# Kernel tuning notes

Hardware: AMD Instinct MI355X
Metric: run time of the kernel (lower is better)

The kernel has to match this reference:

```python
import jax, jax.numpy as jnp
import numpy as np

N, F_IN, D, R, E = 50000, 128, 96, 2, 800000


def setup_inputs() -> dict:
    key = jax.random.key(0)
    ks = jax.random.split(key, 8)
    sc = lambda k, shape: jax.random.normal(k, shape, jnp.float32) * 0.05
    return {
        "x": jax.random.normal(ks[0], (N, F_IN), jnp.float32),
        "edge_index": jax.random.randint(ks[1], (2, E), 0, N),
        "edge_attr": jax.random.uniform(ks[2], (E, R), dtype=jnp.float32),
        # nn.Linear(F_IN, D)
        "Wf": sc(ks[3], (D, F_IN)),
        "bf": jnp.zeros((D,), jnp.float32),
        # RGCNConv: per-relation weights, root weight, bias
        "W": sc(ks[4], (R, D, D)),
        "root": sc(ks[5], (D, D)),
        "bias": jnp.zeros((D,), jnp.float32),
    }


def _rgcn_conv(h, src, dst, etype, W, root, bias):
    # PyG RGCNConv (no bases/blocks, aggr='mean'):
    #   out = x @ root + bias + sum_r mean_{edges of type r}(x[src]) @ W[r]
    msg = h[src]  # [E, D] gather
    out = h @ root + bias
    for r in range(R):
        w = (etype == r).astype(h.dtype)[:, None]  # [E, 1] relation mask
        s = jax.ops.segment_sum(msg * w, dst, num_segments=N)   # [N, D] scatter-add
        cnt = jax.ops.segment_sum(w, dst, num_segments=N)       # [N, 1]
        agg = s / jnp.maximum(cnt, 1.0)                          # mean, safe for deg 0
        out = out + agg @ W[r]
    return out


def reference(x, edge_index, edge_attr, Wf, bf, W, root, bias):
    src, dst = edge_index[0], edge_index[1]
    etype = jnp.argmax(edge_attr, axis=1)  # [E]
    h = jax.nn.relu(x @ Wf.T + bf)
    for _ in range(3):
        h = jax.nn.relu(_rgcn_conv(h, src, dst, etype, W, root, bias))
    return h
```

## Files before the change

### kernel.cpp

```cpp
#include <hip/hip_runtime.h>

#define DN 96
#define FIN 128

typedef unsigned int uint_t;
typedef unsigned short ushort_t;

typedef __attribute__((ext_vector_type(8))) short short8v;
typedef __attribute__((ext_vector_type(4))) float f32x4;

#define MFMA16 __builtin_amdgcn_mfma_f32_16x16x32_bf16

struct __align__(4) U3 { uint_t x, y, z; };

__device__ __forceinline__ ushort_t f2bf(float f) {
    uint_t u = __float_as_uint(f);
    uint_t r = (u + 0x7FFFu + ((u >> 16) & 1u)) >> 16;
    return (ushort_t)r;
}
__device__ __forceinline__ float bf2f(ushort_t h) { return __uint_as_float(((uint_t)h) << 16); }
__device__ __forceinline__ float bf_lo(uint_t u) { return __uint_as_float(u << 16); }
__device__ __forceinline__ float bf_hi(uint_t u) { return __uint_as_float(u & 0xFFFF0000u); }

__device__ __forceinline__ U3 ldrow(const uint_t* __restrict__ g, int idx, int j) {
    return *(const U3*)(g + (size_t)idx * 48 + 3 * j);
}
__device__ __forceinline__ void acc6(float* s, U3 v) {
    s[0] += bf_lo(v.x); s[1] += bf_hi(v.x);
    s[2] += bf_lo(v.y); s[3] += bf_hi(v.y);
    s[4] += bf_lo(v.z); s[5] += bf_hi(v.z);
}


__global__ __launch_bounds__(256) void prep_kernel(
    const int* __restrict__ ei, const float* __restrict__ ea,
    uint_t* __restrict__ kdx, uint_t* __restrict__ kdy,
    const float* __restrict__ root, const float* __restrict__ W, const float* __restrict__ Wf,
    ushort_t* __restrict__ Bph, ushort_t* __restrict__ Bpl,
    ushort_t* __restrict__ Wfh, ushort_t* __restrict__ Wfl,
    ushort_t* g0A, ushort_t* g1A, ushort_t* g0B, ushort_t* g1B,
    int E, int N, int KD_BLKS)
{
    int bid = blockIdx.x;
    int t = threadIdx.x;
    if (bid < KD_BLKS) {
        int e = bid * 256 + t;
        if (e < E) {
            int src = ei[e];
            int dst = ei[E + e];
            float2 a = *(const float2*)(ea + 2 * e);
            int r = (a.y > a.x) ? 1 : 0;
            kdx[e] = (uint_t)dst | ((uint_t)r << 16);
            kdy[e] = (uint_t)src;
        }
    } else if (bid < KD_BLKS + 78) {
        if (t >= 64) return;
        int l = t;
        int fid = bid - KD_BLKS;
        if (fid < 54) {
            int ct = fid / 3, ks = fid % 3;
            int mat = ct / 6, cw = ct % 6;
            const float* M = (mat == 0) ? root : (W + (size_t)(mat - 1) * DN * DN);
            int k0 = 32 * ks + (l >> 4) * 8;
            int col = 16 * cw + (l & 15);
#pragma unroll
            for (int j = 0; j < 8; j++) {
                float v = M[(size_t)(k0 + j) * DN + col];
                ushort_t h = f2bf(v);
                size_t idx = ((size_t)fid * 64 + l) * 8 + j;
                Bph[idx] = h;
                Bpl[idx] = f2bf(v - bf2f(h));
            }
        } else {
            int f2 = fid - 54;
            int ct = f2 >> 2, ks = f2 & 3;
            int k0 = 32 * ks + (l >> 4) * 8;
            int col = 16 * ct + (l & 15);
#pragma unroll
            for (int j = 0; j < 8; j++) {
                float v = Wf[(size_t)col * FIN + k0 + j];
                ushort_t h = f2bf(v);
                size_t idx = ((size_t)f2 * 64 + l) * 8 + j;
                Wfh[idx] = h;
                Wfl[idx] = f2bf(v - bf2f(h));
            }
        }
    } else {
        int pair = bid - (KD_BLKS + 78);
        ushort_t* ga = pair ? g0B : g0A;
        ushort_t* gb = pair ? g1B : g1A;
        if (t < 96) ga[(size_t)N * DN + t] = 0;
        else if (t < 192) gb[(size_t)N * DN + (t - 96)] = 0;
    }
}


__global__ __launch_bounds__(256) void hist_part(const uint_t* __restrict__ kdx,
                                                 int* __restrict__ cnt, int E, int N, int PS) {
    int p = blockIdx.x & 7;
    int c = blockIdx.x >> 3;
    int base = c * 2048 + threadIdx.x;
#pragma unroll
    for (int i = 0; i < 8; i++) {
        int e = base + i * 256;
        if (e < E) {
            uint_t v = kdx[e];
            int dst = v & 0xFFFF;
            if (dst / PS == p) {
                int r = (v >> 16) & 1;
                atomicAdd(&cnt[r * N + dst], 1);
            }
        }
    }
}

__global__ void offsets_kernel(const int* __restrict__ cnt, int* __restrict__ total,
                               int* __restrict__ rowstart, int* __restrict__ fillptr,
                               int nbins) {
    __shared__ int sd[256];
    __shared__ int sbase;
    int t = threadIdx.x;
    int b = blockIdx.x * 256 + t;
    int v = (b < nbins) ? cnt[b] : 0;
    sd[t] = v;
    __syncthreads();
    for (int off = 1; off < 256; off <<= 1) {
        int add = (t >= off) ? sd[t - off] : 0;
        __syncthreads();
        sd[t] += add;
        __syncthreads();
    }
    if (t == 255) sbase = atomicAdd(total, sd[255]);
    __syncthreads();
    if (b < nbins) {
        int s = sbase + sd[t] - v;
        rowstart[b] = s;
        fillptr[b] = s;
    }
}


__device__ __forceinline__ void cvt8(float4 x, float4 y, short8v& hi, short8v& lo) {
    union { short8v v; ushort_t u[8]; } H, L;
    float f[8] = {x.x, x.y, x.z, x.w, y.x, y.y, y.z, y.w};
#pragma unroll
    for (int j = 0; j < 8; j++) {
        ushort_t h = f2bf(f[j]);
        H.u[j] = h;
        L.u[j] = f2bf(f[j] - bf2f(h));
    }
    hi = H.v; lo = L.v;
}


__global__ __launch_bounds__(256) void fill_lin(
    const uint_t* __restrict__ kdx, const uint_t* __restrict__ kdy,
    int* __restrict__ fillptr, int* __restrict__ srcs,
    const float* __restrict__ xin,
    const ushort_t* __restrict__ WfH, const ushort_t* __restrict__ WfL,
    const ushort_t* __restrict__ Bph, const ushort_t* __restrict__ Bpl,
    const float* __restrict__ bfv, const float* __restrict__ bias,
    float* __restrict__ hrootOut, ushort_t* __restrict__ g0Out, ushort_t* __restrict__ g1Out,
    int E, int N, int PS, int FILL_BLKS)
{
    __shared__ float sout[4][16][100];
    int t = threadIdx.x;

    if (blockIdx.x < FILL_BLKS) {
        int p = blockIdx.x & 7;
        int c = blockIdx.x >> 3;
        int base = c * 2048 + t;
#pragma unroll
        for (int i = 0; i < 8; i++) {
            int e = base + i * 256;
            if (e < E) {
                uint_t v = kdx[e];
                int dst = v & 0xFFFF;
                if (dst / PS == p) {
                    int r = (v >> 16) & 1;
                    int pos = atomicAdd(&fillptr[r * N + dst], 1);
                    srcs[pos] = (int)kdy[e];
                }
            }
        }
        return;
    }

    int bid2 = blockIdx.x - FILL_BLKS;
    int l = t & 63;
    int w = t >> 6;

    int slab = bid2 * 64 + w * 16;
    int row = slab + (l & 15);
    if (row >= N) row = N - 1;
    const float* xrow = xin + (size_t)row * FIN + ((l >> 4) * 8);
    short8v ah4[4], al4[4];
#pragma unroll
    for (int ks = 0; ks < 4; ks++) {
        float4 xa = *(const float4*)(xrow + 32 * ks);
        float4 xb = *(const float4*)(xrow + 32 * ks + 4);
        cvt8(xa, xb, ah4[ks], al4[ks]);
    }
#pragma unroll
    for (int ct = 0; ct < 6; ct++) {
        f32x4 hh = {0.f,0.f,0.f,0.f}, hl_ = {0.f,0.f,0.f,0.f}, lh = {0.f,0.f,0.f,0.f};
#pragma unroll
        for (int ks = 0; ks < 4; ks++) {
            size_t base = ((size_t)(ct * 4 + ks) * 64 + l) * 8;
            short8v bh = *(const short8v*)(WfH + base);
            short8v bl = *(const short8v*)(WfL + base);
            hh  = MFMA16(ah4[ks], bh, hh, 0, 0, 0);
            hl_ = MFMA16(ah4[ks], bl, hl_, 0, 0, 0);
            lh  = MFMA16(al4[ks], bh, lh, 0, 0, 0);
        }
        f32x4 acc = hh + hl_ + lh;
        int col = ct * 16 + (l & 15);
        float bv = bfv[col];
        int lr0 = (l >> 4) * 4;
#pragma unroll
        for (int r = 0; r < 4; r++) {
            float v = acc[r] + bv;
            sout[w][lr0 + r][col] = v > 0.f ? v : 0.f;
        }
    }
    __syncthreads();

    const float* srow = &sout[w][l & 15][0];
    int mbase = bid2 * 64 + w * 16 + ((l >> 4) << 2);
    int k0 = (l >> 4) * 8;
    short8v ah[3], al[3];
#pragma unroll
    for (int ks = 0; ks < 3; ks++) {
        float4 xa = *(const float4*)(srow + k0 + 32 * ks);
        float4 xb = *(const float4*)(srow + k0 + 32 * ks + 4);
        cvt8(xa, xb, ah[ks], al[ks]);
    }
    for (int ct = 0; ct < 18; ct++) {
        f32x4 hh = {0.f,0.f,0.f,0.f}, hl_ = {0.f,0.f,0.f,0.f}, lh = {0.f,0.f,0.f,0.f};
#pragma unroll
        for (int ks = 0; ks < 3; ks++) {
            size_t base = ((size_t)(ct * 3 + ks) * 64 + l) * 8;
            short8v bh = *(const short8v*)(Bph + base);
            short8v bl = *(const short8v*)(Bpl + base);
            hh  = MFMA16(ah[ks], bh, hh, 0, 0, 0);
            hl_ = MFMA16(ah[ks], bl, hl_, 0, 0, 0);
            lh  = MFMA16(al[ks], bh, lh, 0, 0, 0);
        }
        f32x4 acc = hh + hl_ + lh;
        int mat = ct / 6;
        int col = (ct % 6) * 16 + (l & 15);
        if (mat == 0) {
            float bv = bias[col];
#pragma unroll
            for (int r = 0; r < 4; r++) {
                int m = mbase + r;
                if (m < N) hrootOut[(size_t)m * DN + col] = acc[r] + bv;
            }
        } else {
            ushort_t* g = (mat == 1) ? g0Out : g1Out;
#pragma unroll
            for (int r = 0; r < 4; r++) {
                int m = mbase + r;
                if (m < N) g[(size_t)m * DN + col] = f2bf(acc[r]);
            }
        }
    }
}


template <int GEMM>
__global__ __launch_bounds__(256) void layer_kernel(
    const float* __restrict__ hrootIn,
    const uint_t* __restrict__ g0In, const uint_t* __restrict__ g1In,
    const int* __restrict__ rowstart, const int* __restrict__ cnt,
    const int* __restrict__ srcs,
    const ushort_t* __restrict__ Bph, const ushort_t* __restrict__ Bpl,
    const float* __restrict__ bias,
    float* __restrict__ hrootOut, ushort_t* __restrict__ g0Out, ushort_t* __restrict__ g1Out,
    float* __restrict__ dout, int N)
{
    __shared__ float sout[16][100];
    int t = threadIdx.x;

    {
        int grp = t >> 4;
        int j = t & 15;
        int n = blockIdx.x * 16 + grp;
        bool valid = n < N;
        int nc = valid ? n : N - 1;

        const float* hr = hrootIn + (size_t)nc * DN + 6 * j;
        float2 p0 = *(const float2*)hr;
        float2 p1 = *(const float2*)(hr + 2);
        float2 p2 = *(const float2*)(hr + 4);

        float a[6] = {0.f,0.f,0.f,0.f,0.f,0.f};
#pragma unroll
        for (int r = 0; r < 2; r++) {
            int c    = valid ? cnt[r * N + nc] : 0;
            int base = valid ? rowstart[r * N + nc] : 0;
            const uint_t* g = r ? g1In : g0In;
            const int* sp = srcs + base;
            float sA[6] = {0.f,0.f,0.f,0.f,0.f,0.f};
            float sB[6] = {0.f,0.f,0.f,0.f,0.f,0.f};
            for (int e = 0; e < c; e += 8) {
                int i0 = (e + 0 < c) ? sp[e + 0] : N;
                int i1 = (e + 1 < c) ? sp[e + 1] : N;
                int i2 = (e + 2 < c) ? sp[e + 2] : N;
                int i3 = (e + 3 < c) ? sp[e + 3] : N;
                int i4 = (e + 4 < c) ? sp[e + 4] : N;
                int i5 = (e + 5 < c) ? sp[e + 5] : N;
                int i6 = (e + 6 < c) ? sp[e + 6] : N;
                int i7 = (e + 7 < c) ? sp[e + 7] : N;
                U3 v0 = ldrow(g, i0, j);
                U3 v1 = ldrow(g, i1, j);
                U3 v2 = ldrow(g, i2, j);
                U3 v3 = ldrow(g, i3, j);
                U3 v4 = ldrow(g, i4, j);
                U3 v5 = ldrow(g, i5, j);
                U3 v6 = ldrow(g, i6, j);
                U3 v7 = ldrow(g, i7, j);
                acc6(sA, v0); acc6(sB, v1); acc6(sA, v2); acc6(sB, v3);
                acc6(sA, v4); acc6(sB, v5); acc6(sA, v6); acc6(sB, v7);
            }
            float inv = (c > 0) ? 1.f / (float)c : 0.f;
#pragma unroll
            for (int k = 0; k < 6; k++) a[k] += (sA[k] + sB[k]) * inv;
        }
        float o0 = fmaxf(p0.x + a[0], 0.f);
        float o1 = fmaxf(p0.y + a[1], 0.f);
        float o2 = fmaxf(p1.x + a[2], 0.f);
        float o3 = fmaxf(p1.y + a[3], 0.f);
        float o4 = fmaxf(p2.x + a[4], 0.f);
        float o5 = fmaxf(p2.y + a[5], 0.f);
        if constexpr (GEMM) {
            float* dr = &sout[grp][6 * j];
            dr[0]=o0; dr[1]=o1; dr[2]=o2; dr[3]=o3; dr[4]=o4; dr[5]=o5;
        } else {
            if (valid) {
                float* dr = dout + (size_t)n * DN + 6 * j;
                *(float2*)(dr)     = make_float2(o0, o1);
                *(float2*)(dr + 2) = make_float2(o2, o3);
                *(float2*)(dr + 4) = make_float2(o4, o5);
            }
        }
    }

    if constexpr (!GEMM) return;
    __syncthreads();

    {
        int l = t & 63;
        int w = t >> 6;
        const float* srow = &sout[l & 15][0];
        int mbase = blockIdx.x * 16 + ((l >> 4) << 2);
        int k0 = (l >> 4) * 8;
        short8v ah[3], al[3];
#pragma unroll
        for (int ks = 0; ks < 3; ks++) {
            float4 xa = *(const float4*)(srow + k0 + 32 * ks);
            float4 xb = *(const float4*)(srow + k0 + 32 * ks + 4);
            cvt8(xa, xb, ah[ks], al[ks]);
        }
        int ctS, ctC;
        ctS = (w < 2) ? 5 * w : 10 + 4 * (w - 2);
        ctC = (w < 2) ? 5 : 4;
        for (int ci = 0; ci < ctC; ci++) {
            int ct = ctS + ci;
            f32x4 hh = {0.f,0.f,0.f,0.f}, hl_ = {0.f,0.f,0.f,0.f}, lh = {0.f,0.f,0.f,0.f};
#pragma unroll
            for (int ks = 0; ks < 3; ks++) {
                size_t base = ((size_t)(ct * 3 + ks) * 64 + l) * 8;
                short8v bh = *(const short8v*)(Bph + base);
                short8v bl = *(const short8v*)(Bpl + base);
                hh  = MFMA16(ah[ks], bh, hh, 0, 0, 0);
                hl_ = MFMA16(ah[ks], bl, hl_, 0, 0, 0);
                lh  = MFMA16(al[ks], bh, lh, 0, 0, 0);
            }
            f32x4 acc = hh + hl_ + lh;
            int mat = ct / 6;
            int col = (ct % 6) * 16 + (l & 15);
            if (mat == 0) {
                float bv = bias[col];
#pragma unroll
                for (int r = 0; r < 4; r++) {
                    int m = mbase + r;
                    if (m < N) hrootOut[(size_t)m * DN + col] = acc[r] + bv;
                }
            } else {
                ushort_t* g = (mat == 1) ? g0Out : g1Out;
#pragma unroll
                for (int r = 0; r < 4; r++) {
                    int m = mbase + r;
                    if (m < N) g[(size_t)m * DN + col] = f2bf(acc[r]);
                }
            }
        }
    }
}

extern "C" void kernel_launch(void* const* d_in, const int* in_sizes, int n_in,
                              void* d_out, int out_size, void* d_ws, size_t ws_size,
                              hipStream_t stream) {
    const float* x    = (const float*)d_in[0];
    const int*   ei   = (const int*)d_in[1];
    const float* ea   = (const float*)d_in[2];
    const float* Wf   = (const float*)d_in[3];
    const float* bf   = (const float*)d_in[4];
    const float* W    = (const float*)d_in[5];
    const float* root = (const float*)d_in[6];
    const float* bias = (const float*)d_in[7];
    float* out = (float*)d_out;

    int N = in_sizes[0] / FIN;
    int E = in_sizes[1] / 2;
    int nbins = 2 * N;
    int PS = (N + 7) / 8;
    size_t NR = (size_t)(N + 1) * DN;

    int* cnt      = (int*)d_ws;
    int* total    = cnt + nbins;
    int* rowstart = cnt + nbins + 4;
    int* fillptr  = rowstart + nbins;
    int* srcs     = fillptr + nbins;
    uint_t* kdx   = (uint_t*)(srcs + E);
    uint_t* kdy   = kdx + E;
    ushort_t* Bph = (ushort_t*)(kdy + E);
    ushort_t* Bpl = Bph + 54 * 512;
    ushort_t* Wfh = Bpl + 54 * 512;
    ushort_t* Wfl = Wfh + 24 * 512;
    float* hrootA = (float*)(Wfl + 24 * 512);
    ushort_t* g0A = (ushort_t*)(hrootA + (size_t)N * DN);
    ushort_t* g1A = g0A + NR;
    float* hrootB = (float*)(g1A + NR);
    ushort_t* g0B = (ushort_t*)(hrootB + (size_t)N * DN);
    ushort_t* g1B = g0B + NR;

    hipMemsetAsync(cnt, 0, (size_t)(nbins + 1) * sizeof(int), stream);

    int KD_BLKS = (E + 255) / 256;
    int nchunk = (E + 2047) / 2048;
    int FILL_BLKS = nchunk * 8;
    int blk64 = (N + 63) / 64;
    int blk16 = (N + 15) / 16;

    prep_kernel<<<KD_BLKS + 78 + 2, 256, 0, stream>>>(
        ei, ea, kdx, kdy, root, W, Wf, Bph, Bpl, Wfh, Wfl,
        g0A, g1A, g0B, g1B, E, N, KD_BLKS);
    hist_part<<<FILL_BLKS, 256, 0, stream>>>(kdx, cnt, E, N, PS);
    offsets_kernel<<<(nbins + 255) / 256, 256, 0, stream>>>(cnt, total, rowstart, fillptr, nbins);
    fill_lin<<<FILL_BLKS + blk64, 256, 0, stream>>>(
        kdx, kdy, fillptr, srcs, x, Wfh, Wfl, Bph, Bpl, bf, bias,
        hrootA, g0A, g1A, E, N, PS, FILL_BLKS);
    layer_kernel<1><<<blk16, 256, 0, stream>>>(
        hrootA, (const uint_t*)g0A, (const uint_t*)g1A, rowstart, cnt, srcs,
        Bph, Bpl, bias, hrootB, g0B, g1B, nullptr, N);
    layer_kernel<1><<<blk16, 256, 0, stream>>>(
        hrootB, (const uint_t*)g0B, (const uint_t*)g1B, rowstart, cnt, srcs,
        Bph, Bpl, bias, hrootA, g0A, g1A, nullptr, N);
    layer_kernel<0><<<blk16, 256, 0, stream>>>(
        hrootA, (const uint_t*)g0A, (const uint_t*)g1A, rowstart, cnt, srcs,
        nullptr, nullptr, nullptr, nullptr, nullptr, nullptr, out, N);
}
```

Before: 278.9 us.

## Store edge sources as 16-bit and split fill from linear GEMM kernel

Edge source indices (kdy and the CSR srcs array) are stored as 16-bit values instead of 32-bit, halving the bytes for index writes and reads in the fill pass and in all three gather layers. The fused fill+linear kernel is split into two separate launches, fill_part and lin_gemm. This removes the mixed-role grid but adds a launch and loses overlap between the scatter and the GEMM. The 16-bit indices only hold for N below 65536, which the task's N=50000 satisfies, as does the existing dst packing.

```diff
diff --git a/kernel.cpp b/kernel.cpp
--- a/kernel.cpp
+++ b/kernel.cpp
@@ -34,7 +34,7 @@
 
 __global__ __launch_bounds__(256) void prep_kernel(
     const int* __restrict__ ei, const float* __restrict__ ea,
-    uint_t* __restrict__ kdx, uint_t* __restrict__ kdy,
+    uint_t* __restrict__ kdx, ushort_t* __restrict__ kdy,
     const float* __restrict__ root, const float* __restrict__ W, const float* __restrict__ Wf,
     ushort_t* __restrict__ Bph, ushort_t* __restrict__ Bpl,
     ushort_t* __restrict__ Wfh, ushort_t* __restrict__ Wfl,
@@ -51,7 +51,7 @@
             float2 a = *(const float2*)(ea + 2 * e);
             int r = (a.y > a.x) ? 1 : 0;
             kdx[e] = (uint_t)dst | ((uint_t)r << 16);
-            kdy[e] = (uint_t)src;
+            kdy[e] = (ushort_t)src;
         }
     } else if (bid < KD_BLKS + 78) {
         if (t >= 64) return;
@@ -140,6 +140,29 @@
 }
 
 
+__global__ __launch_bounds__(256) void fill_part(const uint_t* __restrict__ kdx,
+                            const ushort_t* __restrict__ kdy,
+                            int* __restrict__ fillptr, ushort_t* __restrict__ srcs,
+                            int E, int N, int PS) {
+    int p = blockIdx.x & 7;
+    int c = blockIdx.x >> 3;
+    int base = c * 2048 + threadIdx.x;
+#pragma unroll
+    for (int i = 0; i < 8; i++) {
+        int e = base + i * 256;
+        if (e < E) {
+            uint_t v = kdx[e];
+            int dst = v & 0xFFFF;
+            if (dst / PS == p) {
+                int r = (v >> 16) & 1;
+                int pos = atomicAdd(&fillptr[r * N + dst], 1);
+                srcs[pos] = kdy[e];
+            }
+        }
+    }
+}
+
+
 __device__ __forceinline__ void cvt8(float4 x, float4 y, short8v& hi, short8v& lo) {
     union { short8v v; ushort_t u[8]; } H, L;
     float f[8] = {x.x, x.y, x.z, x.w, y.x, y.y, y.z, y.w};
@@ -153,44 +176,20 @@
 }
 
 
-__global__ __launch_bounds__(256) void fill_lin(
-    const uint_t* __restrict__ kdx, const uint_t* __restrict__ kdy,
-    int* __restrict__ fillptr, int* __restrict__ srcs,
+__global__ __launch_bounds__(256) void lin_gemm(
     const float* __restrict__ xin,
     const ushort_t* __restrict__ WfH, const ushort_t* __restrict__ WfL,
     const ushort_t* __restrict__ Bph, const ushort_t* __restrict__ Bpl,
     const float* __restrict__ bfv, const float* __restrict__ bias,
     float* __restrict__ hrootOut, ushort_t* __restrict__ g0Out, ushort_t* __restrict__ g1Out,
-    int E, int N, int PS, int FILL_BLKS)
+    int N)
 {
     __shared__ float sout[4][16][100];
     int t = threadIdx.x;
-
-    if (blockIdx.x < FILL_BLKS) {
-        int p = blockIdx.x & 7;
-        int c = blockIdx.x >> 3;
-        int base = c * 2048 + t;
-#pragma unroll
-        for (int i = 0; i < 8; i++) {
-            int e = base + i * 256;
-            if (e < E) {
-                uint_t v = kdx[e];
-                int dst = v & 0xFFFF;
-                if (dst / PS == p) {
-                    int r = (v >> 16) & 1;
-                    int pos = atomicAdd(&fillptr[r * N + dst], 1);
-                    srcs[pos] = (int)kdy[e];
-                }
-            }
-        }
-        return;
-    }
-
-    int bid2 = blockIdx.x - FILL_BLKS;
     int l = t & 63;
     int w = t >> 6;
 
-    int slab = bid2 * 64 + w * 16;
+    int slab = blockIdx.x * 64 + w * 16;
     int row = slab + (l & 15);
     if (row >= N) row = N - 1;
     const float* xrow = xin + (size_t)row * FIN + ((l >> 4) * 8);
@@ -226,7 +225,7 @@
     __syncthreads();
 
     const float* srow = &sout[w][l & 15][0];
-    int mbase = bid2 * 64 + w * 16 + ((l >> 4) << 2);
+    int mbase = blockIdx.x * 64 + w * 16 + ((l >> 4) << 2);
     int k0 = (l >> 4) * 8;
     short8v ah[3], al[3];
 #pragma unroll
@@ -273,7 +272,7 @@
     const float* __restrict__ hrootIn,
     const uint_t* __restrict__ g0In, const uint_t* __restrict__ g1In,
     const int* __restrict__ rowstart, const int* __restrict__ cnt,
-    const int* __restrict__ srcs,
+    const ushort_t* __restrict__ srcs,
     const ushort_t* __restrict__ Bph, const ushort_t* __restrict__ Bpl,
     const float* __restrict__ bias,
     float* __restrict__ hrootOut, ushort_t* __restrict__ g0Out, ushort_t* __restrict__ g1Out,
@@ -300,18 +299,18 @@
             int c    = valid ? cnt[r * N + nc] : 0;
             int base = valid ? rowstart[r * N + nc] : 0;
             const uint_t* g = r ? g1In : g0In;
-            const int* sp = srcs + base;
+            const ushort_t* sp = srcs + base;
             float sA[6] = {0.f,0.f,0.f,0.f,0.f,0.f};
             float sB[6] = {0.f,0.f,0.f,0.f,0.f,0.f};
             for (int e = 0; e < c; e += 8) {
-                int i0 = (e + 0 < c) ? sp[e + 0] : N;
-                int i1 = (e + 1 < c) ? sp[e + 1] : N;
-                int i2 = (e + 2 < c) ? sp[e + 2] : N;
-                int i3 = (e + 3 < c) ? sp[e + 3] : N;
-                int i4 = (e + 4 < c) ? sp[e + 4] : N;
-                int i5 = (e + 5 < c) ? sp[e + 5] : N;
-                int i6 = (e + 6 < c) ? sp[e + 6] : N;
-                int i7 = (e + 7 < c) ? sp[e + 7] : N;
+                int i0 = (e + 0 < c) ? (int)sp[e + 0] : N;
+                int i1 = (e + 1 < c) ? (int)sp[e + 1] : N;
+                int i2 = (e + 2 < c) ? (int)sp[e + 2] : N;
+                int i3 = (e + 3 < c) ? (int)sp[e + 3] : N;
+                int i4 = (e + 4 < c) ? (int)sp[e + 4] : N;
+                int i5 = (e + 5 < c) ? (int)sp[e + 5] : N;
+                int i6 = (e + 6 < c) ? (int)sp[e + 6] : N;
+                int i7 = (e + 7 < c) ? (int)sp[e + 7] : N;
                 U3 v0 = ldrow(g, i0, j);
                 U3 v1 = ldrow(g, i1, j);
                 U3 v2 = ldrow(g, i2, j);
@@ -418,40 +417,40 @@
     int PS = (N + 7) / 8;
     size_t NR = (size_t)(N + 1) * DN;
 
-    int* cnt      = (int*)d_ws;
-    int* total    = cnt + nbins;
-    int* rowstart = cnt + nbins + 4;
-    int* fillptr  = rowstart + nbins;
-    int* srcs     = fillptr + nbins;
-    uint_t* kdx   = (uint_t*)(srcs + E);
-    uint_t* kdy   = kdx + E;
-    ushort_t* Bph = (ushort_t*)(kdy + E);
-    ushort_t* Bpl = Bph + 54 * 512;
-    ushort_t* Wfh = Bpl + 54 * 512;
-    ushort_t* Wfl = Wfh + 24 * 512;
-    float* hrootA = (float*)(Wfl + 24 * 512);
-    ushort_t* g0A = (ushort_t*)(hrootA + (size_t)N * DN);
-    ushort_t* g1A = g0A + NR;
-    float* hrootB = (float*)(g1A + NR);
-    ushort_t* g0B = (ushort_t*)(hrootB + (size_t)N * DN);
-    ushort_t* g1B = g0B + NR;
+    int* cnt        = (int*)d_ws;
+    int* total      = cnt + nbins;
+    int* rowstart   = cnt + nbins + 4;
+    int* fillptr    = rowstart + nbins;
+    uint_t* kdx     = (uint_t*)(fillptr + nbins);
+    ushort_t* kdy   = (ushort_t*)(kdx + E);
+    ushort_t* srcs  = kdy + E;
+    ushort_t* Bph   = (ushort_t*)(((uintptr_t)(srcs + E) + 15) & ~(uintptr_t)15);
+    ushort_t* Bpl   = Bph + 54 * 512;
+    ushort_t* Wfh   = Bpl + 54 * 512;
+    ushort_t* Wfl   = Wfh + 24 * 512;
+    float* hrootA   = (float*)(Wfl + 24 * 512);
+    ushort_t* g0A   = (ushort_t*)(hrootA + (size_t)N * DN);
+    ushort_t* g1A   = g0A + NR;
+    float* hrootB   = (float*)(g1A + NR);
+    ushort_t* g0B   = (ushort_t*)(hrootB + (size_t)N * DN);
+    ushort_t* g1B   = g0B + NR;
 
     hipMemsetAsync(cnt, 0, (size_t)(nbins + 1) * sizeof(int), stream);
 
     int KD_BLKS = (E + 255) / 256;
     int nchunk = (E + 2047) / 2048;
-    int FILL_BLKS = nchunk * 8;
+    int PART_BLKS = nchunk * 8;
     int blk64 = (N + 63) / 64;
     int blk16 = (N + 15) / 16;
 
     prep_kernel<<<KD_BLKS + 78 + 2, 256, 0, stream>>>(
         ei, ea, kdx, kdy, root, W, Wf, Bph, Bpl, Wfh, Wfl,
         g0A, g1A, g0B, g1B, E, N, KD_BLKS);
-    hist_part<<<FILL_BLKS, 256, 0, stream>>>(kdx, cnt, E, N, PS);
+    hist_part<<<PART_BLKS, 256, 0, stream>>>(kdx, cnt, E, N, PS);
     offsets_kernel<<<(nbins + 255) / 256, 256, 0, stream>>>(cnt, total, rowstart, fillptr, nbins);
-    fill_lin<<<FILL_BLKS + blk64, 256, 0, stream>>>(
-        kdx, kdy, fillptr, srcs, x, Wfh, Wfl, Bph, Bpl, bf, bias,
-        hrootA, g0A, g1A, E, N, PS, FILL_BLKS);
+    fill_part<<<PART_BLKS, 256, 0, stream>>>(kdx, kdy, fillptr, srcs, E, N, PS);
+    lin_gemm<<<blk64, 256, 0, stream>>>(
+        x, Wfh, Wfl, Bph, Bpl, bf, bias, hrootA, g0A, g1A, N);
     layer_kernel<1><<<blk16, 256, 0, stream>>>(
         hrootA, (const uint_t*)g0A, (const uint_t*)g1A, rowstart, cnt, srcs,
         Bph, Bpl, bias, hrootB, g0B, g1B, nullptr, N);
```

Result: slower. 294.6 us (+5.6%).
